# Kernel tuning notes

Hardware: AMD Instinct MI355X
Metric: run time of the kernel (lower is better)

The kernel has to match this reference:

```python
import jax, jax.numpy as jnp
from jax import lax
import numpy as np

B, INPUT_SIZE, T, H, OUT_LEN = 128, 64, 256, 512, 512


def _lstm_scan(xs, h0, c0, Wih, Whh, bih, bhh):
    """xs: (T, B, in). Returns hidden states per step: (T, B, H).
    PyTorch LSTM gate order: i, f, g, o."""
    b = bih + bhh

    def step(carry, x_t):
        h, c = carry
        gates = x_t @ Wih.T + h @ Whh.T + b  # (B, 4H)
        i, f, g, o = jnp.split(gates, 4, axis=-1)
        c = jax.nn.sigmoid(f) * c + jax.nn.sigmoid(i) * jnp.tanh(g)
        h = jax.nn.sigmoid(o) * jnp.tanh(c)
        return (h, c), h

    _, hs = lax.scan(step, (h0, c0), xs)
    return hs


def setup_inputs() -> dict:
    key = jax.random.key(0)
    ks = jax.random.split(key, 16)
    u = lambda k, shape, fan: jax.random.uniform(k, shape, jnp.float32, -1.0, 1.0) / np.sqrt(fan)
    # xavier_normal_ std for (1, B, H) tensor: sqrt(2 / (B*H + H))
    h_std = np.sqrt(2.0 / ((B + 1) * H)).astype(np.float32)
    return {
        "x": jax.random.normal(ks[0], (B, INPUT_SIZE, T), jnp.float32),
        "h0_enc": h_std * jax.random.normal(ks[1], (B, H), jnp.float32),
        "c0_enc": h_std * jax.random.normal(ks[2], (B, H), jnp.float32),
        "Wih_e": u(ks[3], (4 * H, INPUT_SIZE), H),
        "Whh_e": u(ks[4], (4 * H, H), H),
        "bih_e": u(ks[5], (4 * H,), H),
        "bhh_e": u(ks[6], (4 * H,), H),
        "h0_dec": h_std * jax.random.normal(ks[7], (B, H), jnp.float32),
        "c0_dec": h_std * jax.random.normal(ks[8], (B, H), jnp.float32),
        "Wih_d": u(ks[9], (4 * H, H), H),
        "Whh_d": u(ks[10], (4 * H, H), H),
        "bih_d": u(ks[11], (4 * H,), H),
        "bhh_d": u(ks[12], (4 * H,), H),
        "Wfc": u(ks[13], (OUT_LEN, H * T), H * T),
        "bfc": u(ks[14], (OUT_LEN,), H * T),
    }


def reference(x, h0_enc, c0_enc, Wih_e, Whh_e, bih_e, bhh_e,
              h0_dec, c0_dec, Wih_d, Whh_d, bih_d, bhh_d, Wfc, bfc):
    xs = jnp.transpose(x, (2, 0, 1))  # (T, B, input_size)
    hs_e = _lstm_scan(xs, h0_enc, c0_enc, Wih_e, Whh_e, bih_e, bhh_e)  # (T, B, H)
    encoded = jnp.transpose(hs_e, (1, 2, 0))  # (B, H, T), matches torch layout
    # Decoder consumes encoded[:, :, t] == hs_e[t]
    hs_d = _lstm_scan(hs_e, h0_dec, c0_dec, Wih_d, Whh_d, bih_d, bhh_d)  # (T, B, H)
    flat = jnp.transpose(hs_d, (1, 2, 0)).reshape(x.shape[0], -1)  # (B, H*T)
    decoded = flat @ Wfc.T + bfc  # (B, output_len)
    return encoded, decoded
```

## Files before the change

### kernel.cpp

```cpp
#include <hip/hip_runtime.h>


#define NWG 144

#define OFF_HE  0u
#define OFF_HD  262144u
#define OFF_RD  524288u
#define OFF_WDX 4718592u
#define OFF_XT  6815744u
#define OFF_BAR 11010048u

typedef float f32x4 __attribute__((ext_vector_type(4)));
typedef short s16x8 __attribute__((ext_vector_type(8)));

static __device__ __forceinline__ unsigned short bfu(float f) {
  unsigned u = __builtin_bit_cast(unsigned, f);
  return (unsigned short)((u + 0x7fffu + ((u >> 16) & 1u)) >> 16);
}
static __device__ __forceinline__ float sigm(float x) {
  return 1.0f / (1.0f + exp2f(-1.4426950408889634f * x));
}
static __device__ __forceinline__ float tanh_(float x) {
  return 2.0f / (1.0f + exp2f(-2.8853900817779268f * x)) - 1.0f;
}

static __device__ __forceinline__ void gbar(unsigned* bar, unsigned target) {
  __syncthreads();
  if (threadIdx.x == 0) {
    __builtin_amdgcn_fence(__ATOMIC_RELEASE, "agent");
    __hip_atomic_fetch_add(bar, 1u, __ATOMIC_RELAXED, __HIP_MEMORY_SCOPE_AGENT);
    while (__hip_atomic_load(bar, __ATOMIC_RELAXED, __HIP_MEMORY_SCOPE_AGENT) < target)
      __builtin_amdgcn_s_sleep(1);
    __builtin_amdgcn_fence(__ATOMIC_ACQUIRE, "agent");
  }
  __syncthreads();
}

extern "C" __global__ void __launch_bounds__(256)
lstm_ae(const float* __restrict__ x,
        const float* __restrict__ h0e, const float* __restrict__ c0e,
        const float* __restrict__ wihe, const float* __restrict__ whhe,
        const float* __restrict__ bihe, const float* __restrict__ bhhe,
        const float* __restrict__ h0d, const float* __restrict__ c0d,
        const float* __restrict__ wihd, const float* __restrict__ whhd,
        const float* __restrict__ bihd, const float* __restrict__ bhhd,
        const float* __restrict__ wfc, const float* __restrict__ bfc,
        float* __restrict__ out, char* __restrict__ ws)
{
  extern __shared__ char smem[];
  const int tid  = threadIdx.x;
  const int wave = tid >> 6;
  const int lane = tid & 63;
  const int lg   = lane >> 4;
  const int lc   = lane & 15;
  const int bid  = blockIdx.x;
  const int role = (bid < 64) ? 0 : (bid < 128) ? 1 : 2;

  unsigned short* he   = (unsigned short*)(ws + OFF_HE);
  unsigned short* hd   = (unsigned short*)(ws + OFF_HD);
  unsigned short* ring = (unsigned short*)(ws + OFF_RD);
  unsigned short* wdx  = (unsigned short*)(ws + OFF_WDX);
  unsigned short* xT   = (unsigned short*)(ws + OFF_XT);
  unsigned*       bar  = (unsigned*)(ws + OFF_BAR);
  unsigned ep = 0;

  const int rc   = (role == 0) ? bid : bid - 64;
  const int rowg = rc >> 5, cg = rc & 31;
  const int hc0  = cg * 16;
  const int hc   = hc0 + lc;
  const int row0 = rowg * 64 + wave * 16;

  float  cstate[4] = {0, 0, 0, 0};
  float  bias[4]   = {0, 0, 0, 0};
  s16x8  wihf[4][2];
  f32x4  facc[2][2] = {};

  if (role < 2) {
    const float* W = (role == 0) ? whhe : whhd;
    for (int i = tid; i < 64 * 256; i += 256) {
      int row = i >> 8, kp = i & 255;
      int s = row >> 4, col = row & 15;
      const float* q = W + (s * 512 + hc0 + col) * 512 + kp * 2;
      unsigned v = (unsigned)bfu(q[0]) | ((unsigned)bfu(q[1]) << 16);
      int byte = (((s * 16 + col) * 512 + kp * 2) * 2) ^ ((col & 7) << 4);
      *(unsigned*)(smem + byte) = v;
    }
  }
  if (role == 0) {
    for (int s = 0; s < 4; ++s)
      for (int kx = 0; kx < 2; ++kx) {
        const float* p = wihe + (s * 512 + hc) * 64 + kx * 32 + lg * 8;
        f32x4 a = *(const f32x4*)p, b = *(const f32x4*)(p + 4);
        s16x8 v;
        v[0] = (short)bfu(a[0]); v[1] = (short)bfu(a[1]);
        v[2] = (short)bfu(a[2]); v[3] = (short)bfu(a[3]);
        v[4] = (short)bfu(b[0]); v[5] = (short)bfu(b[1]);
        v[6] = (short)bfu(b[2]); v[7] = (short)bfu(b[3]);
        wihf[s][kx] = v;
      }
    for (int i = tid; i < 1024; i += 256) {
      int b = rowg * 64 + (i >> 4), ch = hc0 + (i & 15);
      he[b * 512 + ch] = bfu(h0e[b * 512 + ch]);
    }
    for (int j = 0; j < 4; ++j) cstate[j] = c0e[(row0 + lg * 4 + j) * 512 + hc];
    for (int s = 0; s < 4; ++s) bias[s] = bihe[s * 512 + hc] + bhhe[s * 512 + hc];
  } else if (role == 1) {
    if (rowg == 0)
      for (int i = tid; i < 64 * 512; i += 256) {
        int row = i >> 9, k = i & 511;
        int s = row >> 4, col = row & 15;
        int n = s * 512 + hc0 + col;
        wdx[n * 512 + k] = bfu(wihd[n * 512 + k]);
      }
    for (int i = tid; i < 1024; i += 256) {
      int b = rowg * 64 + (i >> 4), ch = hc0 + (i & 15);
      hd[65536 + b * 512 + ch] = bfu(h0d[b * 512 + ch]);
    }
    for (int j = 0; j < 4; ++j) cstate[j] = c0d[(row0 + lg * 4 + j) * 512 + hc];
    for (int s = 0; s < 4; ++s) bias[s] = bihd[s * 512 + hc] + bhhd[s * 512 + hc];
  } else {
    int f = bid - 128;
    for (int b = f * 8; b < f * 8 + 8; ++b) {
      int t = tid;
      for (int i0 = 0; i0 < 64; i0 += 8) {
        s16x8 v;
        #pragma unroll
        for (int e = 0; e < 8; ++e) v[e] = (short)bfu(x[(b * 64 + i0 + e) * 256 + t]);
        *(s16x8*)(xT + (t * 128 + b) * 64 + i0) = v;
      }
    }
  }

  gbar(bar, ++ep * NWG);

  auto fc_round = [&](int r) {
    int w = (r - 17) >> 4, s = (r - 17) & 15, slot = w & 1;
    const unsigned short* rb = ring + slot * 1048576;
    int n0 = (bid - 128) * 32;
    #pragma unroll 4
    for (int kk = 0; kk < 16; ++kk) {
      int kw = s * 512 + kk * 32 + lg * 8;
      int h = kw >> 4, tl = kw & 15;
      s16x8 a0 = *(const s16x8*)(rb + ((wave * 32 + lc) * 512 + h) * 16 + tl);
      s16x8 a1 = *(const s16x8*)(rb + ((wave * 32 + 16 + lc) * 512 + h) * 16 + tl);
      #pragma unroll
      for (int nt = 0; nt < 2; ++nt) {
        int n = n0 + nt * 16 + lc;
        const float* wp = wfc + (size_t)n * 131072 + h * 256 + w * 16 + tl;
        f32x4 w0 = *(const f32x4*)wp, w1 = *(const f32x4*)(wp + 4);
        s16x8 bf;
        bf[0] = (short)bfu(w0[0]); bf[1] = (short)bfu(w0[1]);
        bf[2] = (short)bfu(w0[2]); bf[3] = (short)bfu(w0[3]);
        bf[4] = (short)bfu(w1[0]); bf[5] = (short)bfu(w1[1]);
        bf[6] = (short)bfu(w1[2]); bf[7] = (short)bfu(w1[3]);
        facc[0][nt] = __builtin_amdgcn_mfma_f32_16x16x32_bf16(a0, bf, facc[0][nt], 0, 0, 0);
        facc[1][nt] = __builtin_amdgcn_mfma_f32_16x16x32_bf16(a1, bf, facc[1][nt], 0, 0, 0);
      }
    }
  };

  for (int r = 0; r < 272; ++r) {
    if (role == 0) {
      if (r < 256) {
        int t = r;
        const unsigned short* hs   = he + (r & 1) * 65536;
        unsigned short*       hdst = he + ((r + 1) & 1) * 65536;
        f32x4 acc[4];
        #pragma unroll
        for (int s = 0; s < 4; ++s) { f32x4 v = {bias[s], bias[s], bias[s], bias[s]}; acc[s] = v; }
        const unsigned short* arow = hs + (row0 + lc) * 512 + lg * 8;
        #pragma unroll 4
        for (int kk = 0; kk < 16; ++kk) {
          s16x8 a = *(const s16x8*)(arow + kk * 32);
          #pragma unroll
          for (int s = 0; s < 4; ++s) {
            int byte = (((s * 16 + lc) * 512 + kk * 32 + lg * 8) * 2) ^ ((lc & 7) << 4);
            s16x8 b = *(const s16x8*)(smem + byte);
            acc[s] = __builtin_amdgcn_mfma_f32_16x16x32_bf16(a, b, acc[s], 0, 0, 0);
          }
        }
        const unsigned short* xrow = xT + (t * 128 + row0 + lc) * 64 + lg * 8;
        #pragma unroll
        for (int kx = 0; kx < 2; ++kx) {
          s16x8 a = *(const s16x8*)(xrow + kx * 32);
          #pragma unroll
          for (int s = 0; s < 4; ++s)
            acc[s] = __builtin_amdgcn_mfma_f32_16x16x32_bf16(a, wihf[s][kx], acc[s], 0, 0, 0);
        }
        #pragma unroll
        for (int j = 0; j < 4; ++j) {
          int b = row0 + lg * 4 + j;
          float ci = sigm(acc[0][j]), cf = sigm(acc[1][j]);
          float cgg = tanh_(acc[2][j]), co = sigm(acc[3][j]);
          cstate[j] = cf * cstate[j] + ci * cgg;
          float hval = co * tanh_(cstate[j]);
          hdst[b * 512 + hc] = bfu(hval);
          out[b * 131072 + hc * 256 + t] = hval;
        }
      }
    } else if (role == 1) {
      if (r >= 1 && r <= 256) {
        int t = r - 1;
        const unsigned short* hs   = hd + (r & 1) * 65536;
        unsigned short*       hdst = hd + ((r + 1) & 1) * 65536;
        const unsigned short* xs   = he + (r & 1) * 65536;
        f32x4 acc[4];
        #pragma unroll
        for (int s = 0; s < 4; ++s) { f32x4 v = {bias[s], bias[s], bias[s], bias[s]}; acc[s] = v; }
        const unsigned short* arow = hs + (row0 + lc) * 512 + lg * 8;
        #pragma unroll 4
        for (int kk = 0; kk < 16; ++kk) {
          s16x8 a = *(const s16x8*)(arow + kk * 32);
          #pragma unroll
          for (int s = 0; s < 4; ++s) {
            int byte = (((s * 16 + lc) * 512 + kk * 32 + lg * 8) * 2) ^ ((lc & 7) << 4);
            s16x8 b = *(const s16x8*)(smem + byte);
            acc[s] = __builtin_amdgcn_mfma_f32_16x16x32_bf16(a, b, acc[s], 0, 0, 0);
          }
        }
        const unsigned short* xrow = xs + (row0 + lc) * 512 + lg * 8;
        #pragma unroll 4
        for (int kk = 0; kk < 16; ++kk) {
          s16x8 a = *(const s16x8*)(xrow + kk * 32);
          #pragma unroll
          for (int s = 0; s < 4; ++s) {
            const unsigned short* wp = wdx + (size_t)(s * 512 + hc) * 512 + kk * 32 + lg * 8;
            s16x8 b = *(const s16x8*)wp;
            acc[s] = __builtin_amdgcn_mfma_f32_16x16x32_bf16(a, b, acc[s], 0, 0, 0);
          }
        }
        int w = t >> 4, tl = t & 15, slot = w & 1;
        #pragma unroll
        for (int j = 0; j < 4; ++j) {
          int b = row0 + lg * 4 + j;
          float ci = sigm(acc[0][j]), cf = sigm(acc[1][j]);
          float cgg = tanh_(acc[2][j]), co = sigm(acc[3][j]);
          cstate[j] = cf * cstate[j] + ci * cgg;
          float hval = co * tanh_(cstate[j]);
          hdst[b * 512 + hc] = bfu(hval);
          ring[slot * 1048576 + (b * 512 + hc) * 16 + tl] = bfu(hval);
        }
      }
    } else {
      if (r >= 17) fc_round(r);
    }
    gbar(bar, ++ep * NWG);
  }

  if (role == 2) {
    fc_round(272);
    int n0 = (bid - 128) * 32;
    #pragma unroll
    for (int mt = 0; mt < 2; ++mt)
      #pragma unroll
      for (int nt = 0; nt < 2; ++nt)
        #pragma unroll
        for (int j = 0; j < 4; ++j) {
          int b = wave * 32 + mt * 16 + lg * 4 + j;
          int n = n0 + nt * 16 + lc;
          out[16777216 + b * 512 + n] = facc[mt][nt][j] + bfc[n];
        }
  }
}

extern "C" void kernel_launch(void* const* d_in, const int* in_sizes, int n_in,
                              void* d_out, int out_size, void* d_ws, size_t ws_size,
                              hipStream_t stream) {
  (void)in_sizes; (void)n_in; (void)out_size; (void)ws_size;
  const float* x    = (const float*)d_in[0];
  const float* h0e  = (const float*)d_in[1];
  const float* c0e  = (const float*)d_in[2];
  const float* wihe = (const float*)d_in[3];
  const float* whhe = (const float*)d_in[4];
  const float* bihe = (const float*)d_in[5];
  const float* bhhe = (const float*)d_in[6];
  const float* h0d  = (const float*)d_in[7];
  const float* c0d  = (const float*)d_in[8];
  const float* wihd = (const float*)d_in[9];
  const float* whhd = (const float*)d_in[10];
  const float* bihd = (const float*)d_in[11];
  const float* bhhd = (const float*)d_in[12];
  const float* wfc  = (const float*)d_in[13];
  const float* bfc  = (const float*)d_in[14];
  float* out = (float*)d_out;
  char*  ws  = (char*)d_ws;

  hipMemsetAsync(ws + OFF_BAR, 0, 64, stream);
  lstm_ae<<<dim3(NWG), dim3(256), 65536, stream>>>(
      x, h0e, c0e, wihe, whhe, bihe, bhhe,
      h0d, c0d, wihd, whhd, bihd, bhhd, wfc, bfc, out, ws);
}
```

Before: 7.362 ms.

## Replace fenced grid barrier with fence-free barrier and coherent atomic loads/stores

Inside the time loop, the per-step grid barrier no longer issues agent-scope release and acquire fences. Each step now gets its own counter, so blocks compare against a fixed NWG instead of a growing target. Cross-block recurrent state (h buffers and the FC ring) is written and read with relaxed agent-scope atomics so it bypasses non-coherent caches and needs no cache flush or invalidate. The aim is to cut the cost of 272 full-fence barriers. The risk is that relaxed atomics plus a compiler-only barrier may not guarantee ordering, and splitting 16-byte loads into pairs of 8-byte atomics can lose vector-load efficiency.

```diff
diff --git a/kernel.cpp b/kernel.cpp
--- a/kernel.cpp
+++ b/kernel.cpp
@@ -12,6 +12,7 @@
 
 typedef float f32x4 __attribute__((ext_vector_type(4)));
 typedef short s16x8 __attribute__((ext_vector_type(8)));
+typedef unsigned long long u64;
 
 static __device__ __forceinline__ unsigned short bfu(float f) {
   unsigned u = __builtin_bit_cast(unsigned, f);
@@ -24,14 +25,36 @@
   return 2.0f / (1.0f + exp2f(-2.8853900817779268f * x)) - 1.0f;
 }
 
-static __device__ __forceinline__ void gbar(unsigned* bar, unsigned target) {
+static __device__ __forceinline__ s16x8 ld8c(const unsigned short* p) {
+  u64 lo = __hip_atomic_load((const u64*)p,       __ATOMIC_RELAXED, __HIP_MEMORY_SCOPE_AGENT);
+  u64 hi = __hip_atomic_load((const u64*)(p + 4), __ATOMIC_RELAXED, __HIP_MEMORY_SCOPE_AGENT);
+  union { u64 q[2]; s16x8 v; } u;
+  u.q[0] = lo; u.q[1] = hi;
+  return u.v;
+}
+static __device__ __forceinline__ void st2c(unsigned short* p, unsigned short v) {
+  __hip_atomic_store(p, v, __ATOMIC_RELAXED, __HIP_MEMORY_SCOPE_AGENT);
+}
+
+static __device__ __forceinline__ void gbar_full(unsigned* c) {
   __syncthreads();
   if (threadIdx.x == 0) {
     __builtin_amdgcn_fence(__ATOMIC_RELEASE, "agent");
-    __hip_atomic_fetch_add(bar, 1u, __ATOMIC_RELAXED, __HIP_MEMORY_SCOPE_AGENT);
-    while (__hip_atomic_load(bar, __ATOMIC_RELAXED, __HIP_MEMORY_SCOPE_AGENT) < target)
+    __hip_atomic_fetch_add(c, 1u, __ATOMIC_RELAXED, __HIP_MEMORY_SCOPE_AGENT);
+    while (__hip_atomic_load(c, __ATOMIC_RELAXED, __HIP_MEMORY_SCOPE_AGENT) < NWG)
       __builtin_amdgcn_s_sleep(1);
     __builtin_amdgcn_fence(__ATOMIC_ACQUIRE, "agent");
+  }
+  __syncthreads();
+}
+
+static __device__ __forceinline__ void gbar_light(unsigned* c) {
+  __syncthreads();
+  if (threadIdx.x == 0) {
+    __hip_atomic_fetch_add(c, 1u, __ATOMIC_RELAXED, __HIP_MEMORY_SCOPE_AGENT);
+    while (__hip_atomic_load(c, __ATOMIC_RELAXED, __HIP_MEMORY_SCOPE_AGENT) < NWG)
+      __builtin_amdgcn_s_sleep(1);
+    asm volatile("" ::: "memory");
   }
   __syncthreads();
 }
@@ -62,7 +85,6 @@
   unsigned short* wdx  = (unsigned short*)(ws + OFF_WDX);
   unsigned short* xT   = (unsigned short*)(ws + OFF_XT);
   unsigned*       bar  = (unsigned*)(ws + OFF_BAR);
-  unsigned ep = 0;
 
   const int rc   = (role == 0) ? bid : bid - 64;
   const int rowg = rc >> 5, cg = rc & 31;
@@ -131,7 +153,7 @@
     }
   }
 
-  gbar(bar, ++ep * NWG);
+  gbar_full(&bar[0]);
 
   auto fc_round = [&](int r) {
     int w = (r - 17) >> 4, s = (r - 17) & 15, slot = w & 1;
@@ -141,8 +163,8 @@
     for (int kk = 0; kk < 16; ++kk) {
       int kw = s * 512 + kk * 32 + lg * 8;
       int h = kw >> 4, tl = kw & 15;
-      s16x8 a0 = *(const s16x8*)(rb + ((wave * 32 + lc) * 512 + h) * 16 + tl);
-      s16x8 a1 = *(const s16x8*)(rb + ((wave * 32 + 16 + lc) * 512 + h) * 16 + tl);
+      s16x8 a0 = ld8c(rb + ((wave * 32 + lc) * 512 + h) * 16 + tl);
+      s16x8 a1 = ld8c(rb + ((wave * 32 + 16 + lc) * 512 + h) * 16 + tl);
       #pragma unroll
       for (int nt = 0; nt < 2; ++nt) {
         int n = n0 + nt * 16 + lc;
@@ -171,7 +193,7 @@
         const unsigned short* arow = hs + (row0 + lc) * 512 + lg * 8;
         #pragma unroll 4
         for (int kk = 0; kk < 16; ++kk) {
-          s16x8 a = *(const s16x8*)(arow + kk * 32);
+          s16x8 a = ld8c(arow + kk * 32);
           #pragma unroll
           for (int s = 0; s < 4; ++s) {
             int byte = (((s * 16 + lc) * 512 + kk * 32 + lg * 8) * 2) ^ ((lc & 7) << 4);
@@ -194,7 +216,7 @@
           float cgg = tanh_(acc[2][j]), co = sigm(acc[3][j]);
           cstate[j] = cf * cstate[j] + ci * cgg;
           float hval = co * tanh_(cstate[j]);
-          hdst[b * 512 + hc] = bfu(hval);
+          st2c(hdst + b * 512 + hc, bfu(hval));
           out[b * 131072 + hc * 256 + t] = hval;
         }
       }
@@ -210,7 +232,7 @@
         const unsigned short* arow = hs + (row0 + lc) * 512 + lg * 8;
         #pragma unroll 4
         for (int kk = 0; kk < 16; ++kk) {
-          s16x8 a = *(const s16x8*)(arow + kk * 32);
+          s16x8 a = ld8c(arow + kk * 32);
           #pragma unroll
           for (int s = 0; s < 4; ++s) {
             int byte = (((s * 16 + lc) * 512 + kk * 32 + lg * 8) * 2) ^ ((lc & 7) << 4);
@@ -221,7 +243,7 @@
         const unsigned short* xrow = xs + (row0 + lc) * 512 + lg * 8;
         #pragma unroll 4
         for (int kk = 0; kk < 16; ++kk) {
-          s16x8 a = *(const s16x8*)(xrow + kk * 32);
+          s16x8 a = ld8c(xrow + kk * 32);
           #pragma unroll
           for (int s = 0; s < 4; ++s) {
             const unsigned short* wp = wdx + (size_t)(s * 512 + hc) * 512 + kk * 32 + lg * 8;
@@ -237,14 +259,14 @@
           float cgg = tanh_(acc[2][j]), co = sigm(acc[3][j]);
           cstate[j] = cf * cstate[j] + ci * cgg;
           float hval = co * tanh_(cstate[j]);
-          hdst[b * 512 + hc] = bfu(hval);
-          ring[slot * 1048576 + (b * 512 + hc) * 16 + tl] = bfu(hval);
+          st2c(hdst + b * 512 + hc, bfu(hval));
+          st2c(ring + slot * 1048576 + (b * 512 + hc) * 16 + tl, bfu(hval));
         }
       }
     } else {
       if (r >= 17) fc_round(r);
     }
-    gbar(bar, ++ep * NWG);
+    gbar_light(&bar[1 + r]);
   }
 
   if (role == 2) {
@@ -285,7 +307,7 @@
   float* out = (float*)d_out;
   char*  ws  = (char*)d_ws;
 
-  hipMemsetAsync(ws + OFF_BAR, 0, 64, stream);
+  hipMemsetAsync(ws + OFF_BAR, 0, 4096, stream);
   lstm_ae<<<dim3(NWG), dim3(256), 65536, stream>>>(
       x, h0e, c0e, wihe, whhe, bihe, bhhe,
       h0d, c0d, wihd, whhd, bihd, bhhd, wfc, bfc, out, ws);
```

Result: faster. 6.869 ms (-6.7%).
